# Performance work log

Measured on AMD Instinct MI355X. Metric: run time of the kernel, lower is better.

Reference implementation:

```python
import jax, jax.numpy as jnp
import numpy as np

BLOCK_SIZE = 256


def setup_inputs() -> dict:
    key = jax.random.key(0)
    k1, k2, k3, k4 = jax.random.split(key, 4)
    B, T, C, H = 512, 256, 384, 64
    x = jax.random.normal(k1, (B, T, C), dtype=jnp.float32)
    Wk = jax.random.normal(k2, (H, C), dtype=jnp.float32) * (1.0 / np.sqrt(C))
    Wq = jax.random.normal(k3, (H, C), dtype=jnp.float32) * (1.0 / np.sqrt(C))
    Wv = jax.random.normal(k4, (H, C), dtype=jnp.float32) * (1.0 / np.sqrt(C))
    return {"x": x, "Wk": Wk, "Wq": Wq, "Wv": Wv}


def reference(x, Wk, Wq, Wv):
    # x: [B, T, C]; Wk/Wq/Wv: [H, C] (torch nn.Linear weight layout, bias=False)
    B, T, C = x.shape
    H = Wk.shape[0]
    k = jnp.einsum('btc,hc->bth', x, Wk)
    q = jnp.einsum('btc,hc->bth', x, Wq)
    v = jnp.einsum('btc,hc->bth', x, Wv)
    scale = 1.0 / jnp.sqrt(jnp.float32(H))
    scores = jnp.einsum('bqh,bkh->bqk', q, k) * scale  # [B, T, T]
    causal = jnp.tril(jnp.ones((T, T), dtype=bool))
    scores = jnp.where(causal, scores, -jnp.inf)
    weights = jax.nn.softmax(scores, axis=-1)
    # dropout is identity in eval mode
    out = jnp.einsum('bqk,bkh->bqh', weights, v)  # [B, T, H]
    return out
```

## Files before the change

### kernel.cpp

```cpp
#include <hip/hip_runtime.h>
#include <hip/hip_bf16.h>
#include <math.h>

#define TT 256
#define CC 384
#define HH 64

typedef float v4f   __attribute__((ext_vector_type(4)));
typedef short short8 __attribute__((ext_vector_type(8)));

#define MFMA(a, b, c) __builtin_amdgcn_mfma_f32_16x16x32_bf16((a), (b), (c), 0, 0, 0)

__device__ __forceinline__ unsigned short f2bf(float f) {
    unsigned int u = __float_as_uint(f);
    u += 0x7FFFu + ((u >> 16) & 1u);
    return (unsigned short)(u >> 16);
}

__device__ __forceinline__ ushort4 f2bf4(float4 f) {
    union { __hip_bfloat162 h2[2]; ushort4 u4; } cv;
    cv.h2[0] = __float22bfloat162_rn(make_float2(f.x, f.y));
    cv.h2[1] = __float22bfloat162_rn(make_float2(f.z, f.w));
    return cv.u4;
}

#define KLOOP_BARRIER() do {                                   \
    asm volatile("s_waitcnt lgkmcnt(0)" ::: "memory");         \
    __builtin_amdgcn_s_barrier();                              \
    __builtin_amdgcn_sched_barrier(0);                         \
} while (0)

#define QSCALE 0.18033688f

#define XS_OFF 0
#define WS_OFF 5120
#define QF_OFF 12800
#define KF_OFF 29184
#define VF_OFF 45568
#define SM_TOTAL 61952

__global__ __launch_bounds__(512, 2)
void fused_attn(const float* __restrict__ x, const float* __restrict__ Wkp,
                const float* __restrict__ Wqp, const float* __restrict__ Wvp,
                float* __restrict__ out)
{
    __shared__ unsigned short sm[SM_TOTAL];
    unsigned short* x_s = sm + XS_OFF;
    unsigned short* w_s = sm + WS_OFF;

    const int tid  = threadIdx.x;
    const int wave = tid >> 6;
    const int lane = tid & 63;
    const int col  = lane & 15;
    const int quad = lane >> 4;
    const int b    = blockIdx.x;

    const int lr  = tid >> 3;
    const int lc4 = (tid & 7) * 4;

    const float* wqp = Wqp + (size_t)lr * CC + lc4;
    const float* wkp = Wkp + (size_t)lr * CC + lc4;
    const float* wvp = Wvp + (size_t)lr * CC + lc4;

    const int afrag_off = (wave * 16 + col) * 40 + quad * 8;

    #pragma unroll 1
    for (int half = 0; half < 2; ++half) {
        const float* xp = x + ((size_t)b * 256 + half * 128 + lr) * CC + lc4;

        v4f acc[12];
        #pragma unroll
        for (int j = 0; j < 12; ++j) acc[j] = (v4f){0.f, 0.f, 0.f, 0.f};

        float4 xA0 = *(const float4*)(xp);
        float4 xA1 = *(const float4*)(xp + 64 * CC);
        float4 wqA = *(const float4*)(wqp);
        float4 wkA = *(const float4*)(wkp);
        float4 wvA = *(const float4*)(wvp);

        #pragma unroll
        for (int s = 0; s < 12; ++s) {
            float4 xB0, xB1, wqB, wkB, wvB;
            if (s < 11) {
                const int k0 = (s + 1) * 32;
                xB0 = *(const float4*)(xp + k0);
                xB1 = *(const float4*)(xp + 64 * CC + k0);
                wqB = *(const float4*)(wqp + k0);
                wkB = *(const float4*)(wkp + k0);
                wvB = *(const float4*)(wvp + k0);
            }
            KLOOP_BARRIER();
            *(ushort4*)&x_s[lr * 40 + lc4]         = f2bf4(xA0);
            *(ushort4*)&x_s[(lr + 64) * 40 + lc4]  = f2bf4(xA1);
            *(ushort4*)&w_s[lr * 40 + lc4]         = f2bf4(wqA);
            *(ushort4*)&w_s[(64 + lr) * 40 + lc4]  = f2bf4(wkA);
            *(ushort4*)&w_s[(128 + lr) * 40 + lc4] = f2bf4(wvA);
            KLOOP_BARRIER();
            const short8 a = *(const short8*)&x_s[afrag_off];
            #pragma unroll
            for (int nt = 0; nt < 12; ++nt) {
                const short8 bf = *(const short8*)&w_s[(nt * 16 + col) * 40 + quad * 8];
                acc[nt] = MFMA(a, bf, acc[nt]);
            }
            if (s < 11) { xA0 = xB0; xA1 = xB1; wqA = wqB; wkA = wkB; wvA = wvB; }
        }

        #pragma unroll
        for (int nt = 0; nt < 12; ++nt) {
            #pragma unroll
            for (int r = 0; r < 4; ++r) {
                const int rl   = wave * 16 + quad * 4 + r;
                const int trow = half * 128 + rl;
                const int n    = nt * 16 + col;
                float v = acc[nt][r];
                if (nt < 4) {
                    const int h = n;
                    sm[QF_OFF + (trow >> 4) * 1024 + (h >> 3) * 128
                             + (trow & 15) * 8 + (h & 7)] = f2bf(v * QSCALE);
                } else if (nt < 8) {
                    const int h = n - 64;
                    sm[KF_OFF + (trow >> 4) * 1024 + (h >> 3) * 128
                             + (trow & 15) * 8 + (h & 7)] = f2bf(v);
                } else {
                    const int h = n - 128;
                    sm[VF_OFF + (h >> 4) * 4096 + (trow >> 3) * 128
                             + (h & 15) * 8 + (trow & 7)] = f2bf(v);
                }
            }
        }
    }
    __syncthreads();

    unsigned short* Pb = sm + wave * 640;

    #pragma unroll
    for (int mi = 0; mi < 2; ++mi) {
        const int qt = mi ? (15 - wave) : wave;
        const short8 aq0 = *(const short8*)&sm[QF_OFF + qt * 1024 + quad * 128 + col * 8];
        const short8 aq1 = *(const short8*)&sm[QF_OFF + qt * 1024 + 512 + quad * 128 + col * 8];

        float lsum[4];
        v4f oacc[4];
        #pragma unroll
        for (int r = 0; r < 4; ++r) lsum[r] = 0.f;
        #pragma unroll
        for (int hn = 0; hn < 4; ++hn) oacc[hn] = (v4f){0.f, 0.f, 0.f, 0.f};

        const int nch = qt / 2 + 1;
        short8 b00, b01, b10, b11;
        {
            const int t0 = KF_OFF + quad * 128 + col * 8;
            b00 = *(const short8*)&sm[t0];
            b01 = *(const short8*)&sm[t0 + 512];
            b10 = *(const short8*)&sm[t0 + 1024];
            b11 = *(const short8*)&sm[t0 + 1536];
        }
        for (int kc = 0; kc < nch; ++kc) {
            const int kb = kc * 32;
            v4f s0 = (v4f){0.f, 0.f, 0.f, 0.f};
            v4f s1 = (v4f){0.f, 0.f, 0.f, 0.f};
            s0 = MFMA(aq0, b00, s0);
            s0 = MFMA(aq1, b01, s0);
            s1 = MFMA(aq0, b10, s1);
            s1 = MFMA(aq1, b11, s1);
            if (kc + 1 < nch) {
                const int t0 = KF_OFF + (kc + 1) * 2048 + quad * 128 + col * 8;
                b00 = *(const short8*)&sm[t0];
                b01 = *(const short8*)&sm[t0 + 512];
                b10 = *(const short8*)&sm[t0 + 1024];
                b11 = *(const short8*)&sm[t0 + 1536];
            }
            const bool diag = (kc == qt / 2);
            #pragma unroll
            for (int r = 0; r < 4; ++r) {
                const int t = qt * 16 + quad * 4 + r;
                float v0 = s0[r];
                float v1 = s1[r];
                if (diag) {
                    if (kb + col > t)      v0 = -1e30f;
                    if (kb + 16 + col > t) v1 = -1e30f;
                }
                const float p0 = exp2f(v0);
                const float p1 = exp2f(v1);
                lsum[r] += p0 + p1;
                Pb[(quad * 4 + r) * 40 + col]      = f2bf(p0);
                Pb[(quad * 4 + r) * 40 + 16 + col] = f2bf(p1);
            }
            __threadfence_block();
            const short8 ap = *(const short8*)&Pb[col * 40 + quad * 8];
            #pragma unroll
            for (int hn = 0; hn < 4; ++hn) {
                const short8 bv = *(const short8*)&sm[VF_OFF + hn * 4096
                                        + (kc * 4 + quad) * 128 + col * 8];
                oacc[hn] = MFMA(ap, bv, oacc[hn]);
            }
        }

        #pragma unroll
        for (int r = 0; r < 4; ++r) {
            float l = lsum[r];
            l += __shfl_xor(l, 1);
            l += __shfl_xor(l, 2);
            l += __shfl_xor(l, 4);
            l += __shfl_xor(l, 8);
            const int t = qt * 16 + quad * 4 + r;
            const float inv = 1.0f / l;
            float* op = out + ((size_t)b * TT + t) * HH;
            #pragma unroll
            for (int hn = 0; hn < 4; ++hn)
                op[hn * 16 + col] = oacc[hn][r] * inv;
        }
    }
}

extern "C" void kernel_launch(void* const* d_in, const int* in_sizes, int n_in,
                              void* d_out, int out_size, void* d_ws, size_t ws_size,
                              hipStream_t stream) {
    const float* x  = (const float*)d_in[0];
    const float* Wk = (const float*)d_in[1];
    const float* Wq = (const float*)d_in[2];
    const float* Wv = (const float*)d_in[3];
    float* out = (float*)d_out;
    (void)d_ws; (void)ws_size;

    fused_attn<<<dim3(512), dim3(512), 0, stream>>>(x, Wk, Wq, Wv, out);
}
```

Measured before the change: 308.9 us.

## Prepack weights into MFMA fragment layout and load x fragments directly to registers

Adds a small prep kernel that converts Wq/Wk/Wv to bf16 in MFMA B-fragment order in the workspace, so the main loop copies them to LDS without conversion or padding. x is now read by each lane directly in A-fragment order and converted in registers, so the x staging in LDS goes away. Q is kept in registers through an LDS transpose that reuses the weight buffer, which shrinks shared memory and raises the launch bound to 4 blocks per CU. The risks are an extra kernel launch, less coalesced x loads, and higher register pressure under the tighter bound.

```diff
diff --git a/kernel.cpp b/kernel.cpp
--- a/kernel.cpp
+++ b/kernel.cpp
@@ -32,22 +32,35 @@
 
 #define QSCALE 0.18033688f
 
-#define XS_OFF 0
-#define WS_OFF 5120
-#define QF_OFF 12800
-#define KF_OFF 29184
-#define VF_OFF 45568
-#define SM_TOTAL 61952
-
-__global__ __launch_bounds__(512, 2)
-void fused_attn(const float* __restrict__ x, const float* __restrict__ Wkp,
-                const float* __restrict__ Wqp, const float* __restrict__ Wvp,
+#define WST 0
+#define KF  6144
+#define VF  22528
+#define SMU 38912
+
+__global__ __launch_bounds__(512)
+void prep_w(const float* __restrict__ Wkp, const float* __restrict__ Wqp,
+            const float* __restrict__ Wvp, unsigned short* __restrict__ wf)
+{
+    const int idx  = blockIdx.x * 512 + threadIdx.x;
+    const int lane = idx & 63;
+    const int fn   = idx >> 6;
+    const int nt   = fn % 12;
+    const int s    = fn / 12;
+    const int col  = lane & 15, quad = lane >> 4;
+    const float* src = (nt < 4) ? Wqp : (nt < 8) ? Wkp : Wvp;
+    const int h  = (nt & 3) * 16 + col;
+    const int c0 = s * 32 + quad * 8;
+    union { ushort4 u[2]; short8 s8; } pk;
+    pk.u[0] = f2bf4(*(const float4*)(src + (size_t)h * CC + c0));
+    pk.u[1] = f2bf4(*(const float4*)(src + (size_t)h * CC + c0 + 4));
+    *(short8*)(wf + (size_t)idx * 8) = pk.s8;
+}
+
+__global__ __launch_bounds__(512, 4)
+void fused_attn(const float* __restrict__ x, const unsigned short* __restrict__ wf,
                 float* __restrict__ out)
 {
-    __shared__ unsigned short sm[SM_TOTAL];
-    unsigned short* x_s = sm + XS_OFF;
-    unsigned short* w_s = sm + WS_OFF;
-
+    __shared__ unsigned short sm[SMU];
     const int tid  = threadIdx.x;
     const int wave = tid >> 6;
     const int lane = tid & 63;
@@ -55,89 +68,98 @@
     const int quad = lane >> 4;
     const int b    = blockIdx.x;
 
-    const int lr  = tid >> 3;
-    const int lc4 = (tid & 7) * 4;
-
-    const float* wqp = Wqp + (size_t)lr * CC + lc4;
-    const float* wkp = Wkp + (size_t)lr * CC + lc4;
-    const float* wvp = Wvp + (size_t)lr * CC + lc4;
-
-    const int afrag_off = (wave * 16 + col) * 40 + quad * 8;
+    short8 aq0A, aq1A, aq0B, aq1B;
 
     #pragma unroll 1
     for (int half = 0; half < 2; ++half) {
-        const float* xp = x + ((size_t)b * 256 + half * 128 + lr) * CC + lc4;
+        const int rb = half ? (7 - wave) : wave;
+        const float* xrow = x + ((size_t)b * 256 + half * 128 + rb * 16 + col) * CC
+                              + quad * 8;
 
         v4f acc[12];
         #pragma unroll
         for (int j = 0; j < 12; ++j) acc[j] = (v4f){0.f, 0.f, 0.f, 0.f};
 
-        float4 xA0 = *(const float4*)(xp);
-        float4 xA1 = *(const float4*)(xp + 64 * CC);
-        float4 wqA = *(const float4*)(wqp);
-        float4 wkA = *(const float4*)(wkp);
-        float4 wvA = *(const float4*)(wvp);
+        float4 xA0 = *(const float4*)(xrow);
+        float4 xA1 = *(const float4*)(xrow + 4);
+        short8 wA0 = *(const short8*)(wf + (size_t)tid * 8);
+        short8 wA1;
+        if (tid < 256) wA1 = *(const short8*)(wf + (size_t)(512 + tid) * 8);
 
         #pragma unroll
         for (int s = 0; s < 12; ++s) {
-            float4 xB0, xB1, wqB, wkB, wvB;
+            float4 xB0, xB1; short8 wB0, wB1;
             if (s < 11) {
-                const int k0 = (s + 1) * 32;
-                xB0 = *(const float4*)(xp + k0);
-                xB1 = *(const float4*)(xp + 64 * CC + k0);
-                wqB = *(const float4*)(wqp + k0);
-                wkB = *(const float4*)(wkp + k0);
-                wvB = *(const float4*)(wvp + k0);
+                xB0 = *(const float4*)(xrow + (s + 1) * 32);
+                xB1 = *(const float4*)(xrow + (s + 1) * 32 + 4);
+                wB0 = *(const short8*)(wf + ((size_t)(s + 1) * 768 + tid) * 8);
+                if (tid < 256)
+                    wB1 = *(const short8*)(wf + ((size_t)(s + 1) * 768 + 512 + tid) * 8);
             }
             KLOOP_BARRIER();
-            *(ushort4*)&x_s[lr * 40 + lc4]         = f2bf4(xA0);
-            *(ushort4*)&x_s[(lr + 64) * 40 + lc4]  = f2bf4(xA1);
-            *(ushort4*)&w_s[lr * 40 + lc4]         = f2bf4(wqA);
-            *(ushort4*)&w_s[(64 + lr) * 40 + lc4]  = f2bf4(wkA);
-            *(ushort4*)&w_s[(128 + lr) * 40 + lc4] = f2bf4(wvA);
+            *(short8*)&sm[WST + tid * 8] = wA0;
+            if (tid < 256)
+                *(short8*)&sm[WST + (512 + tid) * 8] = wA1;
             KLOOP_BARRIER();
-            const short8 a = *(const short8*)&x_s[afrag_off];
+            union { ushort4 u[2]; short8 s8; } pk;
+            pk.u[0] = f2bf4(xA0); pk.u[1] = f2bf4(xA1);
+            const short8 a = pk.s8;
             #pragma unroll
             for (int nt = 0; nt < 12; ++nt) {
-                const short8 bf = *(const short8*)&w_s[(nt * 16 + col) * 40 + quad * 8];
+                const short8 bf = *(const short8*)&sm[WST + (nt * 64 + lane) * 8];
                 acc[nt] = MFMA(a, bf, acc[nt]);
             }
-            if (s < 11) { xA0 = xB0; xA1 = xB1; wqA = wqB; wkA = wkB; wvA = wvB; }
-        }
-
-        #pragma unroll
-        for (int nt = 0; nt < 12; ++nt) {
+            if (s < 11) { xA0 = xB0; xA1 = xB1; wA0 = wB0; wA1 = wB1; }
+        }
+
+        const int kt = half ? (15 - wave) : wave;
+        #pragma unroll
+        for (int nt = 4; nt < 8; ++nt) {
+            const int h = (nt - 4) * 16 + col;
+            #pragma unroll
+            for (int r = 0; r < 4; ++r)
+                sm[KF + kt * 1024 + (h >> 3) * 128 + (quad * 4 + r) * 8 + (h & 7)]
+                    = f2bf(acc[nt][r]);
+        }
+        #pragma unroll
+        for (int nt = 8; nt < 12; ++nt) {
+            const int h = (nt - 8) * 16 + col;
             #pragma unroll
             for (int r = 0; r < 4; ++r) {
-                const int rl   = wave * 16 + quad * 4 + r;
-                const int trow = half * 128 + rl;
-                const int n    = nt * 16 + col;
-                float v = acc[nt][r];
-                if (nt < 4) {
-                    const int h = n;
-                    sm[QF_OFF + (trow >> 4) * 1024 + (h >> 3) * 128
-                             + (trow & 15) * 8 + (h & 7)] = f2bf(v * QSCALE);
-                } else if (nt < 8) {
-                    const int h = n - 64;
-                    sm[KF_OFF + (trow >> 4) * 1024 + (h >> 3) * 128
-                             + (trow & 15) * 8 + (h & 7)] = f2bf(v);
-                } else {
-                    const int h = n - 128;
-                    sm[VF_OFF + (h >> 4) * 4096 + (trow >> 3) * 128
-                             + (h & 15) * 8 + (trow & 7)] = f2bf(v);
-                }
-            }
-        }
+                const int t = kt * 16 + quad * 4 + r;
+                sm[VF + (h >> 4) * 4096 + (t >> 3) * 128 + (h & 15) * 8 + (t & 7)]
+                    = f2bf(acc[nt][r]);
+            }
+        }
+        __syncthreads();
+        unsigned short* qs = sm + WST + wave * 512;
+        #pragma unroll
+        for (int nt = 0; nt < 2; ++nt)
+            #pragma unroll
+            for (int r = 0; r < 4; ++r)
+                qs[(quad * 4 + r) * 32 + nt * 16 + col] = f2bf(acc[nt][r] * QSCALE);
+        __threadfence_block();
+        const short8 q0 = *(const short8*)&qs[col * 32 + quad * 8];
+        __threadfence_block();
+        #pragma unroll
+        for (int nt = 2; nt < 4; ++nt)
+            #pragma unroll
+            for (int r = 0; r < 4; ++r)
+                qs[(quad * 4 + r) * 32 + (nt - 2) * 16 + col] = f2bf(acc[nt][r] * QSCALE);
+        __threadfence_block();
+        const short8 q1 = *(const short8*)&qs[col * 32 + quad * 8];
+        if (half == 0) { aq0A = q0; aq1A = q1; }
+        else           { aq0B = q0; aq1B = q1; }
     }
     __syncthreads();
 
-    unsigned short* Pb = sm + wave * 640;
+    unsigned short* Pb = sm + WST + wave * 640;
 
     #pragma unroll
     for (int mi = 0; mi < 2; ++mi) {
         const int qt = mi ? (15 - wave) : wave;
-        const short8 aq0 = *(const short8*)&sm[QF_OFF + qt * 1024 + quad * 128 + col * 8];
-        const short8 aq1 = *(const short8*)&sm[QF_OFF + qt * 1024 + 512 + quad * 128 + col * 8];
+        const short8 aq0 = mi ? aq0B : aq0A;
+        const short8 aq1 = mi ? aq1B : aq1A;
 
         float lsum[4];
         v4f oacc[4];
@@ -149,7 +171,7 @@
         const int nch = qt / 2 + 1;
         short8 b00, b01, b10, b11;
         {
-            const int t0 = KF_OFF + quad * 128 + col * 8;
+            const int t0 = KF + quad * 128 + col * 8;
             b00 = *(const short8*)&sm[t0];
             b01 = *(const short8*)&sm[t0 + 512];
             b10 = *(const short8*)&sm[t0 + 1024];
@@ -164,7 +186,7 @@
             s1 = MFMA(aq0, b10, s1);
             s1 = MFMA(aq1, b11, s1);
             if (kc + 1 < nch) {
-                const int t0 = KF_OFF + (kc + 1) * 2048 + quad * 128 + col * 8;
+                const int t0 = KF + (kc + 1) * 2048 + quad * 128 + col * 8;
                 b00 = *(const short8*)&sm[t0];
                 b01 = *(const short8*)&sm[t0 + 512];
                 b10 = *(const short8*)&sm[t0 + 1024];
@@ -190,7 +212,7 @@
             const short8 ap = *(const short8*)&Pb[col * 40 + quad * 8];
             #pragma unroll
             for (int hn = 0; hn < 4; ++hn) {
-                const short8 bv = *(const short8*)&sm[VF_OFF + hn * 4096
+                const short8 bv = *(const short8*)&sm[VF + hn * 4096
                                         + (kc * 4 + quad) * 128 + col * 8];
                 oacc[hn] = MFMA(ap, bv, oacc[hn]);
             }
@@ -221,7 +243,9 @@
     const float* Wq = (const float*)d_in[2];
     const float* Wv = (const float*)d_in[3];
     float* out = (float*)d_out;
-    (void)d_ws; (void)ws_size;
-
-    fused_attn<<<dim3(512), dim3(512), 0, stream>>>(x, Wk, Wq, Wv, out);
-}
+
+    unsigned short* wf = (unsigned short*)d_ws;
+
+    prep_w<<<dim3(18), dim3(512), 0, stream>>>(Wk, Wq, Wv, wf);
+    fused_attn<<<dim3(512), dim3(512), 0, stream>>>(x, wf, out);
+}
```

After: 323.8 us. +4.8%, slower.
